# Kernel optimization log

Measured on AMD Instinct MI355X. Metric: run time of the kernel, lower is better.

## Reference

```python
import jax, jax.numpy as jnp
import numpy as np

N_P = 200000  # points (literals)
N_C = 50000   # constraints (clauses)
D = 64
VOCAB = 400   # max_size**2 = 20**2


def setup_inputs() -> dict:
    key = jax.random.key(0)
    ks = jax.random.split(key, 12)
    s = 0.05
    inp = {}
    inp["embedding"] = jax.random.normal(ks[0], (VOCAB, D)) * s
    inp["cls_bias"] = jnp.zeros((VOCAB,))
    inp["W_cinit"] = jax.random.normal(ks[1], (D, 1)) * s
    inp["b_cinit"] = jnp.zeros((D,))
    # clause LSTMs stacked in c_t order: 0=equi, 1=square, 2=diamond, 3=midpoint
    inp["Wih_c"] = jax.random.normal(ks[2], (4, 4 * D, 4 * D)) * s
    inp["Whh_c"] = jax.random.normal(ks[3], (4, 4 * D, D)) * s
    inp["bih_c"] = jnp.zeros((4, 4 * D))
    inp["bhh_c"] = jnp.zeros((4, 4 * D))
    # point-update LSTM L_u
    inp["Wih_u"] = jax.random.normal(ks[4], (4 * D, D)) * s
    inp["Whh_u"] = jax.random.normal(ks[5], (4 * D, D)) * s
    inp["bih_u"] = jnp.zeros((4 * D,))
    inp["bhh_u"] = jnp.zeros((4 * D,))
    inp["x_p_rand"] = jax.random.uniform(ks[6], (N_P, D))
    inp["y"] = jax.random.randint(ks[7], (N_P,), 0, VOCAB)
    inp["p_t"] = jax.random.randint(ks[8], (N_P,), 0, 2)
    inp["c_t"] = jax.random.randint(ks[9], (N_C,), 0, 4)
    inp["p2c"] = jax.random.randint(ks[10], (N_C, 4), 0, N_P)
    inp["num_iters"] = 2
    return inp


def _lstm_cell(x, h, c, Wih, Whh, bih, bhh):
    # torch nn.LSTM single-step cell, gate order (i, f, g, o)
    gates = x @ Wih.T + bih + h @ Whh.T + bhh
    i, f, g, o = jnp.split(gates, 4, axis=-1)
    c_new = jax.nn.sigmoid(f) * c + jax.nn.sigmoid(i) * jnp.tanh(g)
    h_new = jax.nn.sigmoid(o) * jnp.tanh(c_new)
    return h_new, c_new


def reference(embedding, cls_bias, W_cinit, b_cinit, Wih_c, Whh_c, bih_c, bhh_c,
              Wih_u, Whh_u, bih_u, bhh_u, x_p_rand, y, p_t, c_t, p2c, num_iters):
    n_p, d = x_p_rand.shape
    n_c = c_t.shape[0]
    fixed = (p_t != 0)[:, None]  # fixed points keep their embedding
    x_p = jnp.where(fixed, embedding[y], x_p_rand)
    c_init = W_cinit[:, 0] + b_cinit  # C_init(ones(1))
    x_c = jnp.broadcast_to(c_init, (n_c, d))
    x_p_h = jnp.zeros_like(x_p)
    x_c_h = jnp.zeros_like(x_c)
    sel = jax.nn.one_hot(c_t, 4, dtype=x_p.dtype)  # [n_c, 4] clause-type selector
    flat_p2c = p2c.reshape(-1)
    for _ in range(num_iters):
        # LC: gather the 4 points of each constraint
        vars_ = x_p[p2c]  # [n_c, 4, d]
        vars_full = vars_.reshape(n_c, 4 * d)
        vars_mid = vars_.at[:, 3].set(0.0).reshape(n_c, 4 * d)  # midpoint zeros 4th slot
        hs, cs = [], []
        for tp in range(4):
            inp_t = vars_mid if tp == 3 else vars_full
            h_t, c_new = _lstm_cell(inp_t, x_c, x_c_h, Wih_c[tp], Whh_c[tp], bih_c[tp], bhh_c[tp])
            hs.append(h_t)
            cs.append(c_new)
        hs = jnp.stack(hs)  # [4, n_c, d]
        cs = jnp.stack(cs)
        x_c = jnp.einsum('tnd,nt->nd', hs, sel)
        x_c_h = jnp.einsum('tnd,nt->nd', cs, sel)
        # CL: msg = adj.T @ x_c, i.e. scatter-add x_c over incidence edges
        msg = jax.ops.segment_sum(jnp.repeat(x_c, 4, axis=0), flat_p2c, num_segments=n_p)
        h_u, c_u = _lstm_cell(msg, x_p, x_p_h, Wih_u, Whh_u, bih_u, bhh_u)
        # only variable points are updated; fixed points keep old state
        x_p = jnp.where(fixed, x_p, h_u)
        x_p_h = jnp.where(fixed, x_p_h, c_u)
    logits = x_p @ embedding.T + cls_bias  # tied classifier
    return logits
```

## Files before the change

kernel.cpp:

```cpp
#include <hip/hip_runtime.h>
#include <hip/hip_bf16.h>

#define DD 64
#define GG 256

typedef __attribute__((ext_vector_type(8))) __bf16 bfrag;
typedef __attribute__((ext_vector_type(4))) float f32x4;

__device__ __forceinline__ float sigmf(float x){ return 1.f/(1.f+__expf(-x)); }
__device__ __forceinline__ float tanhfast(float x){ return 1.f - 2.f/(__expf(2.f*x)+1.f); }
__device__ __forceinline__ short bf16c(float f){
  __hip_bfloat16 h = __float2bfloat16(f);
  return *reinterpret_cast<short*>(&h);
}

__global__ void k_setup(
    const float* __restrict__ Wihc, const float* __restrict__ Whhc,
    const float* __restrict__ Wihu, const float* __restrict__ Whhu,
    const float* __restrict__ emb, const float* __restrict__ Wci,
    const float* __restrict__ bci, const float* __restrict__ xpr,
    const int* __restrict__ y, const int* __restrict__ pt,
    const int* __restrict__ ct, const int* __restrict__ p2c,
    short* __restrict__ Wc_lay, short* __restrict__ Wu_lay,
    short* __restrict__ E_lay,
    short* __restrict__ xp_bf, short* __restrict__ xc_bf,
    int* __restrict__ tlist, int* __restrict__ cnt,
    int* __restrict__ vlist, int* __restrict__ cnt2,
    int* __restrict__ deg, int NP, int NC)
{
  int b = blockIdx.x;
  const int t = threadIdx.x;
  if (b < 1280){
    int idx = b*256 + t;
    int tp = idx / 81920, r = idx % 81920;
    int ks = r / 8192;  int r2 = r % 8192;
    int nt = r2 / 512;  int r3 = r2 % 512;
    int lr = r3 / 32;   int r4 = r3 % 32;
    int lk = r4 / 8,    e  = r4 % 8;
    int g = nt*16 + lr, k = ks*32 + lk*8 + e;
    float v = (k < 256) ? Wihc[((size_t)tp*256+g)*256 + k]
                        : Whhc[((size_t)tp*256+g)*64 + (k-256)];
    Wc_lay[idx] = bf16c(v);
    return;
  }
  b -= 1280;
  if (b < 128){
    int idx = b*256 + t;
    int ks = idx / 8192; int r2 = idx % 8192;
    int nt = r2 / 512;   int r3 = r2 % 512;
    int lr = r3 / 32;    int r4 = r3 % 32;
    int lk = r4 / 8,     e  = r4 % 8;
    int g = nt*16 + lr, k = ks*32 + lk*8 + e;
    float v = (k < 64) ? Wihu[g*64 + k] : Whhu[g*64 + (k-64)];
    Wu_lay[idx] = bf16c(v);
    return;
  }
  b -= 128;
  if (b < 100){
    int idx = b*256 + t;
    int ks = idx / 12800; int r = idx % 12800;
    int nt = r / 512;     int r3 = r % 512;
    int lr = r3 / 32;     int r4 = r3 % 32;
    int lk = r4 / 8,      e  = r4 % 8;
    int v = nt*16 + lr, k = ks*32 + lk*8 + e;
    E_lay[idx] = bf16c(emb[v*64 + k]);
    return;
  }
  b -= 100;
  int nbP4 = (NP*4 + 255) >> 8;
  if (b < nbP4){
    int i = b*256 + t;
    if (i < NP*4){
      int p = i >> 2, ch = i & 3;
      const float* src = (pt[p]!=0) ? (emb + (size_t)y[p]*DD + ch*16)
                                    : (xpr + (size_t)p*DD + ch*16);
      short o[16];
      #pragma unroll
      for (int f4=0; f4<4; ++f4){
        float4 v = ((const float4*)src)[f4];
        o[f4*4+0]=bf16c(v.x); o[f4*4+1]=bf16c(v.y); o[f4*4+2]=bf16c(v.z); o[f4*4+3]=bf16c(v.w);
      }
      *(uint4*)(xp_bf + (size_t)p*DD + ch*16)     = *(uint4*)&o[0];
      *(uint4*)(xp_bf + (size_t)p*DD + ch*16 + 8) = *(uint4*)&o[8];
    }
    return;
  }
  b -= nbP4;
  int nbC4 = (NC*4 + 255) >> 8;
  if (b < nbC4){
    int i = b*256 + t;
    if (i < NC*4){
      int c = i >> 2, ch = i & 3;
      short o[16];
      #pragma unroll
      for (int d=0; d<16; ++d) o[d] = bf16c(Wci[ch*16+d] + bci[ch*16+d]);
      *(uint4*)(xc_bf + (size_t)c*DD + ch*16)     = *(uint4*)&o[0];
      *(uint4*)(xc_bf + (size_t)c*DD + ch*16 + 8) = *(uint4*)&o[8];
    }
    return;
  }
  b -= nbC4;
  int nbCl = (NC + 255) >> 8;
  if (b < nbCl){
    int c = b*256 + t;
    int lane = t & 63;
    int tp = (c < NC) ? ct[c] : -1;
    unsigned long long lt = (lane == 63) ? ~0ull >> 1 : ((1ull << lane) - 1ull);
    #pragma unroll
    for (int ty=0; ty<4; ++ty){
      unsigned long long m = __ballot(tp==ty);
      if (m == 0ull) continue;
      int nw = __popcll(m), rank = __popcll(m & lt);
      int leader = __ffsll((long long)m) - 1;
      int base = 0;
      if (lane == leader) base = atomicAdd(cnt + ty, nw);
      base = __shfl(base, leader);
      if (tp == ty) tlist[ty*NC + base + rank] = c;
    }
    return;
  }
  b -= nbCl;
  int nbCp = (NP + 255) >> 8;
  if (b < nbCp){
    int p = b*256 + t;
    int lane = t & 63;
    bool var = (p < NP) && (pt[p]==0);
    unsigned long long lt = (lane == 63) ? ~0ull >> 1 : ((1ull << lane) - 1ull);
    unsigned long long m = __ballot(var);
    if (m){
      int nw = __popcll(m), rank = __popcll(m & lt);
      int leader = __ffsll((long long)m) - 1;
      int base = 0;
      if (lane == leader) base = atomicAdd(cnt2, nw);
      base = __shfl(base, leader);
      if (var) vlist[base + rank] = p;
    }
    return;
  }
  b -= nbCp;
  {
    int e = b*256 + t;
    if (e < NC*4) atomicAdd(deg + p2c[e], 1);
  }
}

__global__ void k_rowstart(const int* __restrict__ deg, int* __restrict__ rowstart,
                           int* __restrict__ gtot, int NP){
  int p = blockIdx.x*256 + threadIdx.x;
  int lane = threadIdx.x & 63;
  int d = (p < NP) ? deg[p] : 0;
  int pre = d;
  #pragma unroll
  for (int off=1; off<64; off<<=1){
    int v = __shfl_up(pre, off);
    if (lane >= off) pre += v;
  }
  int tot = __shfl(pre, 63);
  int base = 0;
  if (lane == 63 && tot) base = atomicAdd(gtot, tot);
  base = __shfl(base, 63);
  if (p < NP) rowstart[p] = base + pre - d;
}
__global__ void k_fill(const int* __restrict__ p2c, const int* __restrict__ rowstart,
                       int* __restrict__ cursor, int* __restrict__ elist, int NE){
  int e = blockIdx.x*256 + threadIdx.x;
  if (e >= NE) return;
  int p = p2c[e];
  int pos = atomicAdd(cursor + p, 1);
  elist[rowstart[p] + pos] = e >> 2;
}

__launch_bounds__(256)
__global__ void k_clause(const short* __restrict__ Wc_lay,
                         const float* __restrict__ bih, const float* __restrict__ bhh,
                         const short* __restrict__ xp_bf,
                         short* __restrict__ xc_bf, float* __restrict__ xch,
                         const int* __restrict__ p2c, const int* __restrict__ tlist,
                         const int* __restrict__ cnt, int NC, int first){
  __shared__ __align__(16) short As[64][328];
  int tp, n, base;
  {
    const int c0=cnt[0], c1=cnt[1], c2=cnt[2], c3=cnt[3];
    int b = blockIdx.x;
    const int t0=(c0+63)>>6;
    if (b < t0){ tp=0; n=c0; base=b<<6; }
    else { b-=t0; const int t1=(c1+63)>>6;
      if (b < t1){ tp=1; n=c1; base=b<<6; }
      else { b-=t1; const int t2=(c2+63)>>6;
        if (b < t2){ tp=2; n=c2; base=b<<6; }
        else { b-=t2; const int t3=(c3+63)>>6;
          if (b < t3){ tp=3; n=c3; base=b<<6; } else return; } } }
  }
  const int t = threadIdx.x;
  {
    int row = t >> 2, ch = t & 3;
    int idx = base + row;
    int c = (idx < n) ? tlist[tp*NC + idx] : -1;
    #pragma unroll
    for (int slot=0; slot<5; ++slot){
      uint4 v0 = make_uint4(0,0,0,0), v1 = make_uint4(0,0,0,0);
      const short* src = nullptr;
      if (c >= 0){
        if (slot < 4){
          if (!(tp==3 && slot==3)){
            int p = p2c[c*4 + slot];
            src = xp_bf + (size_t)p*DD + ch*16;
          }
        } else src = xc_bf + (size_t)c*DD + ch*16;
      }
      if (src){ v0 = *(const uint4*)src; v1 = *(const uint4*)(src+8); }
      *(uint4*)&As[row][slot*64 + ch*16 + 0] = v0;
      *(uint4*)&As[row][slot*64 + ch*16 + 8] = v1;
    }
  }
  __syncthreads();
  const int lane = t & 63, w = t >> 6;
  const int lr = lane & 15, lk = lane >> 4;
  f32x4 acc[16];
  #pragma unroll
  for (int i=0;i<16;i++) acc[i] = (f32x4){0.f,0.f,0.f,0.f};
  const short* wb = Wc_lay + (size_t)tp*81920 + (lr*4 + lk)*8;
  #pragma unroll
  for (int ks=0; ks<10; ++ks){
    bfrag a = *(const bfrag*)&As[w*16 + lr][ks*32 + lk*8];
    #pragma unroll
    for (int nt=0; nt<16; ++nt){
      bfrag bv = *(const bfrag*)(wb + (ks*16 + nt)*512);
      acc[nt] = __builtin_amdgcn_mfma_f32_16x16x32_bf16(a, bv, acc[nt], 0, 0, 0);
    }
  }
  #pragma unroll
  for (int r=0; r<4; ++r){
    int idx = base + w*16 + lk*4 + r;
    if (idx >= n) continue;
    int c = tlist[tp*NC + idx];
    #pragma unroll
    for (int q=0; q<4; ++q){
      int d = lr + 16*q;
      float gi = acc[q][r]    + bih[tp*GG + d]       + bhh[tp*GG + d];
      float gf = acc[4+q][r]  + bih[tp*GG + 64 + d]  + bhh[tp*GG + 64 + d];
      float gn = acc[8+q][r]  + bih[tp*GG + 128 + d] + bhh[tp*GG + 128 + d];
      float go = acc[12+q][r] + bih[tp*GG + 192 + d] + bhh[tp*GG + 192 + d];
      float cold = first ? 0.f : xch[(size_t)c*DD + d];
      float cn = sigmf(gf)*cold + sigmf(gi)*tanhfast(gn);
      float hn = sigmf(go)*tanhfast(cn);
      xc_bf[(size_t)c*DD + d] = bf16c(hn);
      xch[(size_t)c*DD + d]   = cn;
    }
  }
}

__launch_bounds__(256)
__global__ void k_point(const short* __restrict__ Wu_lay,
                        const float* __restrict__ bihu, const float* __restrict__ bhhu,
                        const short* __restrict__ xc_bf,
                        const int* __restrict__ rowstart, const int* __restrict__ deg,
                        const int* __restrict__ elist, const int* __restrict__ vlist,
                        const int* __restrict__ nvp,
                        short* __restrict__ xp_bf, float* __restrict__ xph,
                        int NP, int first){
  const int nv = nvp[0];
  const int base = blockIdx.x*64;
  if (base >= nv) return;
  __shared__ __align__(16) short As[64][136];
  const int t = threadIdx.x;
  {
    int row = t >> 2, ch = t & 3;
    int idx = base + row;
    int gr = (idx < nv) ? vlist[idx] : -1;
    float s[16];
    #pragma unroll
    for (int z=0; z<16; ++z) s[z] = 0.f;
    uint4 xv0 = make_uint4(0,0,0,0), xv1 = make_uint4(0,0,0,0);
    if (gr >= 0){
      int rs = rowstart[gr], dg = deg[gr];
      for (int j=0; j<dg; ++j){
        int c = elist[rs + j];
        const uint4* xcp = (const uint4*)(xc_bf + (size_t)c*DD + ch*16);
        uint4 u0 = xcp[0], u1 = xcp[1];
        uint ua[8] = {u0.x,u0.y,u0.z,u0.w,u1.x,u1.y,u1.z,u1.w};
        #pragma unroll
        for (int i2=0;i2<8;i2++){
          s[i2*2]   += __uint_as_float(ua[i2] << 16);
          s[i2*2+1] += __uint_as_float(ua[i2] & 0xffff0000u);
        }
      }
      const uint4* xpp = (const uint4*)(xp_bf + (size_t)gr*DD + ch*16);
      xv0 = xpp[0]; xv1 = xpp[1];
    }
    short os[16];
    #pragma unroll
    for (int z=0; z<16; ++z) os[z] = bf16c(s[z]);
    *(uint4*)&As[row][ch*16 + 0] = *(uint4*)&os[0];
    *(uint4*)&As[row][ch*16 + 8] = *(uint4*)&os[8];
    *(uint4*)&As[row][64 + ch*16 + 0] = xv0;
    *(uint4*)&As[row][64 + ch*16 + 8] = xv1;
  }
  __syncthreads();
  const int lane = t & 63, w = t >> 6;
  const int lr = lane & 15, lk = lane >> 4;
  f32x4 acc[16];
  #pragma unroll
  for (int i=0;i<16;i++) acc[i] = (f32x4){0.f,0.f,0.f,0.f};
  const short* wb = Wu_lay + (lr*4 + lk)*8;
  #pragma unroll
  for (int ks=0; ks<4; ++ks){
    bfrag a = *(const bfrag*)&As[w*16 + lr][ks*32 + lk*8];
    #pragma unroll
    for (int nt=0; nt<16; ++nt){
      bfrag bv = *(const bfrag*)(wb + (ks*16 + nt)*512);
      acc[nt] = __builtin_amdgcn_mfma_f32_16x16x32_bf16(a, bv, acc[nt], 0, 0, 0);
    }
  }
  #pragma unroll
  for (int r=0; r<4; ++r){
    int idx = base + w*16 + lk*4 + r;
    if (idx >= nv) continue;
    int m = vlist[idx];
    #pragma unroll
    for (int q=0; q<4; ++q){
      int d = lr + 16*q;
      float gi = acc[q][r]    + bihu[d]       + bhhu[d];
      float gf = acc[4+q][r]  + bihu[64 + d]  + bhhu[64 + d];
      float gn = acc[8+q][r]  + bihu[128 + d] + bhhu[128 + d];
      float go = acc[12+q][r] + bihu[192 + d] + bhhu[192 + d];
      float cold = first ? 0.f : xph[(size_t)idx*DD + d];
      float cn = sigmf(gf)*cold + sigmf(gi)*tanhfast(gn);
      float hn = sigmf(go)*tanhfast(cn);
      xp_bf[(size_t)m*DD + d] = bf16c(hn);
      xph[(size_t)idx*DD + d] = cn;
    }
  }
}

#define ST 212
__launch_bounds__(256)
__global__ void k_logits(const short* __restrict__ xp_bf, const short* __restrict__ E_lay,
                         const float* __restrict__ cbias,
                         float* __restrict__ out, int NP, int V){
  const int base = blockIdx.x*64;
  __shared__ __align__(16) char smem[64*ST*4];
  short (*As)[72] = (short (*)[72])smem;
  float (*T)[ST]  = (float (*)[ST])smem;
  const int t = threadIdx.x;
  {
    int row = t >> 2, ch = t & 3;
    int gr = base + row;
    uint4 v0 = make_uint4(0,0,0,0), v1 = make_uint4(0,0,0,0);
    if (gr < NP){
      const uint4* src = (const uint4*)(xp_bf + (size_t)gr*DD + ch*16);
      v0 = src[0]; v1 = src[1];
    }
    *(uint4*)&As[row][ch*16 + 0] = v0;
    *(uint4*)&As[row][ch*16 + 8] = v1;
  }
  __syncthreads();
  const int lane = t & 63, w = t >> 6;
  const int lr = lane & 15, lk = lane >> 4;
  f32x4 acc[25];
  #pragma unroll
  for (int i=0;i<25;i++) acc[i] = (f32x4){0.f,0.f,0.f,0.f};
  const short* wb = E_lay + (lr*4 + lk)*8;
  #pragma unroll
  for (int ks=0; ks<2; ++ks){
    bfrag a = *(const bfrag*)&As[w*16 + lr][ks*32 + lk*8];
    #pragma unroll
    for (int nt=0; nt<25; ++nt){
      bfrag bv = *(const bfrag*)(wb + (ks*25 + nt)*512);
      acc[nt] = __builtin_amdgcn_mfma_f32_16x16x32_bf16(a, bv, acc[nt], 0, 0, 0);
    }
  }
  #pragma unroll
  for (int chunk=0; chunk<2; ++chunk){
    const int nt0 = chunk ? 13 : 0;
    const int nt1 = chunk ? 25 : 13;
    const int cb  = nt0*16;
    const int nc4 = chunk ? 48 : 52;
    __syncthreads();
    #pragma unroll
    for (int nt=nt0; nt<nt1; ++nt){
      float cbv = cbias[nt*16 + lr];
      #pragma unroll
      for (int r=0; r<4; ++r)
        T[w*16 + lk*4 + r][nt*16 + lr - cb] = acc[nt][r] + cbv;
    }
    __syncthreads();
    #pragma unroll
    for (int rr=0; rr<16; ++rr){
      int row = w*16 + rr;
      int m = base + row;
      if (m < NP && lane < nc4)
        *(float4*)(out + (size_t)m*V + cb + lane*4) = *(float4*)&T[row][lane*4];
    }
  }
}

extern "C" void kernel_launch(void* const* d_in, const int* in_sizes, int n_in,
                              void* d_out, int out_size, void* d_ws, size_t ws_size,
                              hipStream_t stream){
  const float* emb   = (const float*)d_in[0];
  const float* cbias = (const float*)d_in[1];
  const float* Wci   = (const float*)d_in[2];
  const float* bci   = (const float*)d_in[3];
  const float* Wihc  = (const float*)d_in[4];
  const float* Whhc  = (const float*)d_in[5];
  const float* bihc  = (const float*)d_in[6];
  const float* bhhc  = (const float*)d_in[7];
  const float* Wihu  = (const float*)d_in[8];
  const float* Whhu  = (const float*)d_in[9];
  const float* bihu  = (const float*)d_in[10];
  const float* bhhu  = (const float*)d_in[11];
  const float* xpr   = (const float*)d_in[12];
  const int* y    = (const int*)d_in[13];
  const int* pt   = (const int*)d_in[14];
  const int* ct   = (const int*)d_in[15];
  const int* p2c  = (const int*)d_in[16];
  const int NP = in_sizes[13];
  const int NC = in_sizes[15];
  const int V  = in_sizes[1];
  const int NE = NC*4;

  char* w = (char*)d_ws;
  auto alloc = [&](size_t bytes)->char*{ char* p = w; w += (bytes + 255) & ~255ull; return p; };
  short* xp_bf = (short*)alloc((size_t)NP*DD*2);
  float* xph   = (float*)alloc((size_t)NP*DD*4);
  short* xc_bf = (short*)alloc((size_t)NC*DD*2);
  float* xch   = (float*)alloc((size_t)NC*DD*4);
  int*   tlist = (int*)alloc((size_t)4*NC*4);
  short* Wc_lay= (short*)alloc((size_t)327680*2);
  short* Wu_lay= (short*)alloc((size_t)32768*2);
  short* E_lay = (short*)alloc((size_t)25600*2);
  int*   deg     = (int*)alloc((size_t)NP*4);
  int*   cursor  = (int*)alloc((size_t)NP*4);
  int*   ctr     = (int*)alloc(256);
  int*   rowstart= (int*)alloc((size_t)NP*4);
  int*   elist   = (int*)alloc((size_t)NE*4);
  int*   vlist   = (int*)alloc((size_t)NP*4);
  int* cnt  = ctr;
  int* cnt2 = ctr + 16;
  int* gtot = ctr + 17;

  const int NB   = (NP + 255)/256;
  const int nbP4 = (NP*4 + 255)/256;
  const int nbC4 = (NC*4 + 255)/256;
  const int nbCl = (NC + 255)/256;
  const int nbCp = NB;
  const int nbE  = (NE + 255)/256;
  const int g_setup = 1280 + 128 + 100 + nbP4 + nbC4 + nbCl + nbCp + nbE;

  hipMemsetAsync(deg, 0, (size_t)NP*8 + 256, stream);
  k_setup<<<g_setup, 256, 0, stream>>>(Wihc, Whhc, Wihu, Whhu, emb, Wci, bci, xpr,
                                       y, pt, ct, p2c,
                                       Wc_lay, Wu_lay, E_lay,
                                       xp_bf, xc_bf,
                                       tlist, cnt, vlist, cnt2, deg, NP, NC);
  k_rowstart<<<NB, 256, 0, stream>>>(deg, rowstart, gtot, NP);
  k_fill<<<nbE, 256, 0, stream>>>(p2c, rowstart, cursor, elist, NE);

  const int ctiles = (NC+63)/64 + 3;
  const int num_iters = 2;
  for (int it=0; it<num_iters; ++it){
    k_clause<<<ctiles, 256, 0, stream>>>(Wc_lay, bihc, bhhc, xp_bf, xc_bf, xch,
                                         p2c, tlist, cnt, NC, it==0);
    k_point<<<(NP+63)/64, 256, 0, stream>>>(Wu_lay, bihu, bhhu, xc_bf,
                                            rowstart, deg, elist, vlist, cnt2,
                                            xp_bf, xph, NP, it==0);
  }
  k_logits<<<(NP+63)/64, 256, 0, stream>>>(xp_bf, E_lay, cbias, (float*)d_out, NP, V);
}
```

Baseline: 441.1 us.

## Swap MFMA operands in logits kernel to write output directly without LDS

The logits kernel now puts the embedding as the A operand and the point features as B. Each lane's accumulator then holds four consecutive vocab entries for one point and can be stored as a float4 straight to global memory. This drops the LDS staging buffer and its barriers. The vocab dimension is also split across a second grid axis of 5 tiles each, giving more blocks with fewer accumulators. The trade-off is that each output row is written by strided per-lane float4 stores rather than fully coalesced row stores, and point features are re-read once per vocab group.

Result: slower. 456.6 us (+3.5%).

```diff
diff --git a/kernel.cpp b/kernel.cpp
--- a/kernel.cpp
+++ b/kernel.cpp
@@ -333,65 +333,42 @@
   }
 }
 
-#define ST 212
 __launch_bounds__(256)
 __global__ void k_logits(const short* __restrict__ xp_bf, const short* __restrict__ E_lay,
                          const float* __restrict__ cbias,
                          float* __restrict__ out, int NP, int V){
-  const int base = blockIdx.x*64;
-  __shared__ __align__(16) char smem[64*ST*4];
-  short (*As)[72] = (short (*)[72])smem;
-  float (*T)[ST]  = (float (*)[ST])smem;
   const int t = threadIdx.x;
-  {
-    int row = t >> 2, ch = t & 3;
-    int gr = base + row;
-    uint4 v0 = make_uint4(0,0,0,0), v1 = make_uint4(0,0,0,0);
-    if (gr < NP){
-      const uint4* src = (const uint4*)(xp_bf + (size_t)gr*DD + ch*16);
-      v0 = src[0]; v1 = src[1];
-    }
-    *(uint4*)&As[row][ch*16 + 0] = v0;
-    *(uint4*)&As[row][ch*16 + 8] = v1;
-  }
-  __syncthreads();
   const int lane = t & 63, w = t >> 6;
   const int lr = lane & 15, lk = lane >> 4;
-  f32x4 acc[25];
-  #pragma unroll
-  for (int i=0;i<25;i++) acc[i] = (f32x4){0.f,0.f,0.f,0.f};
-  const short* wb = E_lay + (lr*4 + lk)*8;
+  const int p = blockIdx.x*64 + w*16 + lr;
+  const int nt0 = blockIdx.y*5;
+  const bool ok = p < NP;
+  f32x4 acc[5];
+  #pragma unroll
+  for (int j=0;j<5;j++) acc[j] = (f32x4){0.f,0.f,0.f,0.f};
+  const short* ab = E_lay + (lr*4 + lk)*8;
   #pragma unroll
   for (int ks=0; ks<2; ++ks){
-    bfrag a = *(const bfrag*)&As[w*16 + lr][ks*32 + lk*8];
-    #pragma unroll
-    for (int nt=0; nt<25; ++nt){
-      bfrag bv = *(const bfrag*)(wb + (ks*25 + nt)*512);
-      acc[nt] = __builtin_amdgcn_mfma_f32_16x16x32_bf16(a, bv, acc[nt], 0, 0, 0);
-    }
-  }
-  #pragma unroll
-  for (int chunk=0; chunk<2; ++chunk){
-    const int nt0 = chunk ? 13 : 0;
-    const int nt1 = chunk ? 25 : 13;
-    const int cb  = nt0*16;
-    const int nc4 = chunk ? 48 : 52;
-    __syncthreads();
-    #pragma unroll
-    for (int nt=nt0; nt<nt1; ++nt){
-      float cbv = cbias[nt*16 + lr];
-      #pragma unroll
-      for (int r=0; r<4; ++r)
-        T[w*16 + lk*4 + r][nt*16 + lr - cb] = acc[nt][r] + cbv;
-    }
-    __syncthreads();
-    #pragma unroll
-    for (int rr=0; rr<16; ++rr){
-      int row = w*16 + rr;
-      int m = base + row;
-      if (m < NP && lane < nc4)
-        *(float4*)(out + (size_t)m*V + cb + lane*4) = *(float4*)&T[row][lane*4];
-    }
+    bfrag b;
+    if (ok) b = *(const bfrag*)(xp_bf + (size_t)p*DD + ks*32 + lk*8);
+    else    b = (bfrag){0,0,0,0,0,0,0,0};
+    #pragma unroll
+    for (int j=0; j<5; ++j){
+      bfrag a = *(const bfrag*)(ab + (ks*25 + nt0 + j)*512);
+      acc[j] = __builtin_amdgcn_mfma_f32_16x16x32_bf16(a, b, acc[j], 0, 0, 0);
+    }
+  }
+  if (!ok) return;
+  #pragma unroll
+  for (int j=0; j<5; ++j){
+    int v = (nt0 + j)*16 + lk*4;
+    float4 cb = *(const float4*)(cbias + v);
+    float4 r;
+    r.x = acc[j][0] + cb.x;
+    r.y = acc[j][1] + cb.y;
+    r.z = acc[j][2] + cb.z;
+    r.w = acc[j][3] + cb.w;
+    *(float4*)(out + (size_t)p*V + v) = r;
   }
 }
 
@@ -466,5 +443,7 @@
                                             rowstart, deg, elist, vlist, cnt2,
                                             xp_bf, xph, NP, it==0);
   }
-  k_logits<<<(NP+63)/64, 256, 0, stream>>>(xp_bf, E_lay, cbias, (float*)d_out, NP, V);
-}
+  const int ngv = (V/16 + 4)/5;
+  k_logits<<<dim3((NP+63)/64, ngv), 256, 0, stream>>>(xp_bf, E_lay, cbias,
+                                                      (float*)d_out, NP, V);
+}
```
